# Optimization experiments

Hardware: AMD Instinct MI355X
Metric: run time of the kernel (lower is better)

## Reference

```python
import jax, jax.numpy as jnp
import numpy as np

B, N, C1 = 4, 4096, 58
K = 32
RADIUS = 0.3
CIN = C1 + 6  # xyz(3) + centered grouped_xyz(3) + feature(C1)
OUT_DIMS = [64, 64, 128]
EPS = 1e-5


def setup_inputs() -> dict:
    key = jax.random.key(0)
    ks = jax.random.split(key, 8)
    inp = {
        "feature": jax.random.normal(ks[0], (B, N, C1), dtype=jnp.float32),
        "xyz": jax.random.uniform(ks[1], (B, N, 3), dtype=jnp.float32),
    }
    dims = [CIN] + OUT_DIMS
    for i in range(len(OUT_DIMS)):
        inp[f"W{i}"] = jax.random.normal(ks[2 + i], (dims[i + 1], dims[i]), dtype=jnp.float32) * 0.05
        inp[f"g{i}"] = jnp.ones((dims[i + 1],), dtype=jnp.float32)
        inp[f"b{i}"] = jnp.zeros((dims[i + 1],), dtype=jnp.float32)
    return inp


def ball_query(xyz, radius, k):
    # xyz: (B,N,3) -> grouped neighbor indices (B,N,K), repo semantics:
    # indices with dist > radius set to N, sorted, first K taken, pads replaced by first valid index.
    n = xyz.shape[1]
    sq = jnp.sum((xyz[:, :, None, :] - xyz[:, None, :, :]) ** 2, axis=-1)  # (B,N,N)
    ar = jnp.arange(n, dtype=jnp.int32)[None, None, :]
    inds = jnp.where(sq > radius * radius, n, ar)
    inds = jnp.sort(inds, axis=-1)[:, :, :k]  # (B,N,K)
    first = inds[:, :, :1]
    return jnp.where(inds == n, first, inds)


def group_norm(x, gamma, beta, groups):
    # x: (B,C,K,N); normalize per (group of channels x all spatial)
    b, c, k, n = x.shape
    xg = x.reshape(b, groups, -1)
    mu = jnp.mean(xg, axis=-1, keepdims=True)
    var = jnp.var(xg, axis=-1, keepdims=True)
    xg = (xg - mu) * jax.lax.rsqrt(var + EPS)
    x = xg.reshape(b, c, k, n)
    return x * gamma[None, :, None, None] + beta[None, :, None, None]


def reference(feature, xyz, W0, g0, b0, W1, g1, b1, W2, g2, b2):
    inds = ball_query(xyz, RADIUS, K)  # (B,N,K) int
    gather = jax.vmap(lambda arr, idx: arr[idx])  # per-batch fancy gather
    grouped_xyz = gather(xyz, inds) - xyz[:, :, None, :]        # (B,N,K,3) centered
    grouped_feat = gather(feature, inds)                        # (B,N,K,C1)
    center = jnp.broadcast_to(xyz[:, :, None, :], (B, N, K, 3))  # repeated query xyz
    new_points = jnp.concatenate([center, grouped_xyz, grouped_feat], axis=-1)  # (B,N,K,CIN)

    x = new_points  # layout handled inside einsum: torch permute(0,3,2,1) -> (B,C,K,N)
    params = [(W0, g0, b0), (W1, g1, b1), (W2, g2, b2)]
    first = True
    for (w, g, b_), od in zip(params, OUT_DIMS):
        if first:
            x = jnp.einsum('bnkc,oc->bokn', x, w)  # conv1x1, no bias
            first = False
        else:
            x = jnp.einsum('bikn,oi->bokn', x, w)
        x = group_norm(x, g, b_, od // 32)
        x = jax.nn.relu(x)
    return jnp.max(x, axis=2)  # (B, C2, N)
```

## Files before the change

### kernel.cpp

```cpp
#include <hip/hip_runtime.h>
#include <stdint.h>

#define B_ 4
#define N_ 4096
#define C1_ 58
#define K_ 32
#define EPS_ 1e-5f

typedef __attribute__((ext_vector_type(8))) short bf16x8;
typedef __attribute__((ext_vector_type(4))) float f32x4;

static __device__ __forceinline__ float bf2f(unsigned short u){
  return __uint_as_float(((unsigned int)u) << 16);
}
static __device__ __forceinline__ unsigned short f2bf(float f){
  unsigned int x = __float_as_uint(f);
  x = (x + 0x7FFFu + ((x >> 16) & 1u)) >> 16;
  return (unsigned short)x;
}

__global__ __launch_bounds__(256) void ball_kernel(const float* __restrict__ xyz,
                                                   int* __restrict__ inds){
  const int wid  = (blockIdx.x * 256 + threadIdx.x) >> 6;
  const int lane = threadIdx.x & 63;
  const int b = wid >> 12;
  const int n = wid & (N_ - 1);
  const float* xb = xyz + (size_t)b * N_ * 3;
  const float qx = xb[n*3+0], qy = xb[n*3+1], qz = xb[n*3+2];
  const float R2 = (float)(0.3 * 0.3);
  int* outp = inds + (size_t)wid * K_;
  int cnt = 0;
  int first = -1;
  for (int j0 = 0; j0 < N_ && cnt < K_; j0 += 64){
    const int j = j0 + lane;
    float dx = xb[j*3+0] - qx;
    float dy = xb[j*3+1] - qy;
    float dz = xb[j*3+2] - qz;
    float s = __fadd_rn(__fadd_rn(__fmul_rn(dx,dx), __fmul_rn(dy,dy)), __fmul_rn(dz,dz));
    bool p = (s <= R2);
    unsigned long long mask = __ballot(p);
    if (p){
      int pos = cnt + __popcll(mask & ((1ull << lane) - 1ull));
      if (pos < K_) outp[pos] = j;
    }
    if (first < 0 && mask) first = j0 + __builtin_ctzll(mask);
    cnt += __popcll(mask);
  }
  if (lane < K_ && lane >= cnt) outp[lane] = first;
}

__global__ __launch_bounds__(256)
void pq_kernel(const float* __restrict__ feature, const float* __restrict__ xyz,
               const float* __restrict__ W0g, const float* __restrict__ W2g,
               float* __restrict__ P, unsigned short* __restrict__ Q,
               unsigned short* __restrict__ W2bf)
{
  __shared__ float W0l[64 * 65];
  __shared__ float vql[32][64];
  const int t = threadIdx.x, bid = blockIdx.x;

  if (bid == 0){
    for (int i = t; i < 128 * 64; i += 256) W2bf[i] = f2bf(W2g[i]);
  }
  #pragma unroll
  for (int i = 0; i < 16; ++i){
    int idx = i * 256 + t;
    W0l[(idx >> 6) * 65 + (idx & 63)] = W0g[idx];
  }
  const int gpt0 = bid * 32;
  const int b = gpt0 >> 12;
  const size_t pb = (size_t)b * N_;
  #pragma unroll
  for (int i = 0; i < 8; ++i){
    int task = i * 256 + t;
    int r = task >> 6, c = task & 63;
    int n = (gpt0 + r) & (N_ - 1);
    float val = 0.f;
    if (c < 3)       val = xyz[(pb + n) * 3 + c];
    else if (c < 61) val = feature[(pb + n) * C1_ + (c - 3)];
    vql[r][c] = val;
  }
  __syncthreads();

  const int o = t & 63;
  const int r0 = t >> 6;
  #pragma unroll
  for (int it = 0; it < 8; ++it){
    int r = r0 + it * 4;
    float q0 = 0.f, q1 = 0.f;
    #pragma unroll
    for (int i = 0; i < 60; i += 2){
      q0 = fmaf(W0l[o*65 + 3 + i],     vql[r][i],     q0);
      q1 = fmaf(W0l[o*65 + 3 + i + 1], vql[r][i + 1], q1);
    }
    q0 = fmaf(W0l[o*65 + 3 + 60], vql[r][60], q0);
    float qv = q0 + q1;
    float p = 0.f;
    #pragma unroll
    for (int c = 0; c < 3; ++c)
      p = fmaf(W0l[o*65 + c] - W0l[o*65 + c + 3], vql[r][c], p);
    size_t gpt = (size_t)gpt0 + r;
    P[gpt * 64 + o] = p;
    Q[gpt * 64 + o] = f2bf(qv);
  }
}

__global__ __launch_bounds__(256)
void stats0_kernel(const int* __restrict__ inds, const float* __restrict__ P,
                   const unsigned short* __restrict__ Q, float* __restrict__ partials)
{
  const int t = threadIdx.x, bid = blockIdx.x;
  const size_t row0 = (size_t)bid * 1024;
  const int c8 = t & 7;
  float s = 0.f, q = 0.f;
  for (int i = 0; i < 32; ++i){
    size_t task = (size_t)i * 256 + t;
    size_t row = row0 + (task >> 3);
    int idx = inds[row];
    size_t pt = row >> 5;
    size_t qpt = ((row >> 17) << 12) + idx;
    const float4* pp = (const float4*)(P + pt * 64 + c8 * 8);
    float4 pa = pp[0], pb = pp[1];
    bf16x8 qv = *(const bf16x8*)(Q + qpt * 64 + c8 * 8);
    float pv[8] = {pa.x, pa.y, pa.z, pa.w, pb.x, pb.y, pb.z, pb.w};
    #pragma unroll
    for (int j = 0; j < 8; ++j){
      float y = pv[j] + bf2f((unsigned short)qv[j]);
      s += y; q = fmaf(y, y, q);
    }
  }
  s += __shfl_xor(s, 1, 64);  q += __shfl_xor(q, 1, 64);
  s += __shfl_xor(s, 2, 64);  q += __shfl_xor(q, 2, 64);
  s += __shfl_xor(s, 8, 64);  q += __shfl_xor(q, 8, 64);
  s += __shfl_xor(s, 16, 64); q += __shfl_xor(q, 16, 64);
  s += __shfl_xor(s, 32, 64); q += __shfl_xor(q, 32, 64);
  const int lane = t & 63, w = t >> 6;
  float* out = partials + ((size_t)bid * 4 + w) * 4;
  if (lane == 0){ out[0] = s; out[1] = q; }
  if (lane == 4){ out[2] = s; out[3] = q; }
}

template<int DEPTH>
__global__ __launch_bounds__(512)
void conv_chain(const int* __restrict__ inds, const float* __restrict__ P,
                const unsigned short* __restrict__ Q,
                const float* __restrict__ sc0, const float* __restrict__ sb0,
                const float* __restrict__ W1g, const unsigned short* __restrict__ W2bf,
                const float* __restrict__ sc1, const float* __restrict__ sb1,
                float* __restrict__ partials, float* __restrict__ ymax,
                float* __restrict__ ymin)
{
  constexpr int NGF = (DEPTH == 2) ? 4 : 2;
  constexpr int NG2 = NGF * 2;
  __shared__ unsigned short W1l[64 * 64];
  __shared__ unsigned short Xl[256 * 64];
  __shared__ float spart[8][NG2];

  const int t = threadIdx.x, bid = blockIdx.x;
  const size_t row0 = (size_t)bid * 256;
  const int b = bid >> 9;
  const int lane = t & 63, w = t >> 6;
  const int col = lane & 15, quad = lane >> 4;
  const int c8 = t & 7;

  float s0r[8], b0r[8];
  #pragma unroll
  for (int j = 0; j < 8; ++j){
    s0r[j] = sc0[b * 64 + c8 * 8 + j];
    b0r[j] = sb0[b * 64 + c8 * 8 + j];
  }
  float s1r[4], b1r[4];
  if constexpr (DEPTH == 2){
    #pragma unroll
    for (int nt = 0; nt < 4; ++nt){
      s1r[nt] = sc1[b * 64 + nt * 16 + col];
      b1r[nt] = sb1[b * 64 + nt * 16 + col];
    }
  }

  {
    int ch = t >> 3, c = t & 7;
    const float* wr = W1g + ch * 64 + c * 8;
    bf16x8 v;
    #pragma unroll
    for (int j = 0; j < 8; ++j) v[j] = (short)f2bf(wr[j]);
    *(bf16x8*)&W1l[ch * 64 + ((c ^ (ch & 7)) * 8)] = v;
  }

  #pragma unroll
  for (int i = 0; i < 4; ++i){
    int task = i * 512 + t;
    int r = task >> 3;
    size_t row = row0 + r;
    int idx = inds[row];
    size_t pt = row >> 5;
    size_t qpt = ((row >> 17) << 12) + idx;
    const float4* pp = (const float4*)(P + pt * 64 + c8 * 8);
    float4 pa = pp[0], pb = pp[1];
    bf16x8 qv = *(const bf16x8*)(Q + qpt * 64 + c8 * 8);
    float pv[8] = {pa.x, pa.y, pa.z, pa.w, pb.x, pb.y, pb.z, pb.w};
    bf16x8 v;
    #pragma unroll
    for (int j = 0; j < 8; ++j){
      float y = pv[j] + bf2f((unsigned short)qv[j]);
      float a = fmaf(y, s0r[j], b0r[j]);
      a = fmaxf(a, 0.f);
      v[j] = (short)f2bf(a);
    }
    *(bf16x8*)&Xl[r * 64 + ((c8 ^ (r & 7)) * 8)] = v;
  }
  __syncthreads();

  bf16x8 afr[2][2];
  #pragma unroll
  for (int mi = 0; mi < 2; ++mi){
    int r = w * 32 + mi * 16 + col;
    #pragma unroll
    for (int kt = 0; kt < 2; ++kt)
      afr[mi][kt] = *(const bf16x8*)&Xl[r * 64 + (((kt * 4 + quad) ^ (r & 7)) * 8)];
  }
  f32x4 acc1[2][4];
  #pragma unroll
  for (int mi = 0; mi < 2; ++mi)
    #pragma unroll
    for (int nt = 0; nt < 4; ++nt) acc1[mi][nt] = (f32x4){0.f,0.f,0.f,0.f};
  #pragma unroll
  for (int kt = 0; kt < 2; ++kt)
    #pragma unroll
    for (int nt = 0; nt < 4; ++nt){
      int ch = nt * 16 + col;
      bf16x8 bfr = *(const bf16x8*)&W1l[ch * 64 + (((kt * 4 + quad) ^ (ch & 7)) * 8)];
      #pragma unroll
      for (int mi = 0; mi < 2; ++mi)
        acc1[mi][nt] = __builtin_amdgcn_mfma_f32_16x16x32_bf16(afr[mi][kt], bfr, acc1[mi][nt], 0, 0, 0);
    }

  float sg[NGF], qg[NGF];
  #pragma unroll
  for (int g = 0; g < NGF; ++g){ sg[g] = 0.f; qg[g] = 0.f; }

  if constexpr (DEPTH == 1){
    #pragma unroll
    for (int mi = 0; mi < 2; ++mi)
      #pragma unroll
      for (int nt = 0; nt < 4; ++nt)
        #pragma unroll
        for (int rg = 0; rg < 4; ++rg){
          float y = acc1[mi][nt][rg];
          sg[nt >> 1] += y;
          qg[nt >> 1] = fmaf(y, y, qg[nt >> 1]);
        }
  } else {
    #pragma unroll
    for (int mi = 0; mi < 2; ++mi)
      #pragma unroll
      for (int nt = 0; nt < 4; ++nt)
        #pragma unroll
        for (int rg = 0; rg < 4; ++rg){
          int r = w * 32 + mi * 16 + quad * 4 + rg;
          int ch = nt * 16 + col;
          float v = fmaf(acc1[mi][nt][rg], s1r[nt], b1r[nt]);
          v = fmaxf(v, 0.f);
          Xl[r * 64 + (((ch >> 3) ^ (r & 7)) * 8) + (ch & 7)] = f2bf(v);
        }

    #pragma unroll
    for (int mi = 0; mi < 2; ++mi){
      int r = w * 32 + mi * 16 + col;
      #pragma unroll
      for (int kt = 0; kt < 2; ++kt)
        afr[mi][kt] = *(const bf16x8*)&Xl[r * 64 + (((kt * 4 + quad) ^ (r & 7)) * 8)];
    }
    f32x4 acc2[2][8];
    #pragma unroll
    for (int mi = 0; mi < 2; ++mi)
      #pragma unroll
      for (int nt = 0; nt < 8; ++nt) acc2[mi][nt] = (f32x4){0.f,0.f,0.f,0.f};
    #pragma unroll
    for (int kt = 0; kt < 2; ++kt)
      #pragma unroll
      for (int nt = 0; nt < 8; ++nt){
        int ch = nt * 16 + col;
        bf16x8 bfr = *(const bf16x8*)&W2bf[ch * 64 + (kt * 4 + quad) * 8];
        #pragma unroll
        for (int mi = 0; mi < 2; ++mi)
          acc2[mi][nt] = __builtin_amdgcn_mfma_f32_16x16x32_bf16(afr[mi][kt], bfr, acc2[mi][nt], 0, 0, 0);
      }

    #pragma unroll
    for (int mi = 0; mi < 2; ++mi)
      #pragma unroll
      for (int nt = 0; nt < 8; ++nt)
        #pragma unroll
        for (int rg = 0; rg < 4; ++rg){
          float y = acc2[mi][nt][rg];
          sg[nt >> 1] += y;
          qg[nt >> 1] = fmaf(y, y, qg[nt >> 1]);
        }

    float cmx[8], cmn[8];
    #pragma unroll
    for (int nt = 0; nt < 8; ++nt){
      float mx = acc2[0][nt][0], mn = acc2[0][nt][0];
      #pragma unroll
      for (int mi = 0; mi < 2; ++mi)
        #pragma unroll
        for (int rg = 0; rg < 4; ++rg){
          float y = acc2[mi][nt][rg];
          mx = fmaxf(mx, y); mn = fminf(mn, y);
        }
      mx = fmaxf(mx, __shfl_xor(mx, 16, 64));
      mx = fmaxf(mx, __shfl_xor(mx, 32, 64));
      mn = fminf(mn, __shfl_xor(mn, 16, 64));
      mn = fminf(mn, __shfl_xor(mn, 32, 64));
      cmx[nt] = mx; cmn[nt] = mn;
    }
    if (quad == 0){
      size_t pt = (row0 >> 5) + w;
      #pragma unroll
      for (int nt = 0; nt < 8; ++nt){
        ymax[pt * 128 + nt * 16 + col] = cmx[nt];
        ymin[pt * 128 + nt * 16 + col] = cmn[nt];
      }
    }
  }

  #pragma unroll
  for (int g = 0; g < NGF; ++g){
    #pragma unroll
    for (int off = 32; off > 0; off >>= 1){
      sg[g] += __shfl_down(sg[g], off, 64);
      qg[g] += __shfl_down(qg[g], off, 64);
    }
  }
  if (lane == 0){
    #pragma unroll
    for (int g = 0; g < NGF; ++g){
      spart[w][g * 2 + 0] = sg[g];
      spart[w][g * 2 + 1] = qg[g];
    }
  }
  __syncthreads();
  if (t < NG2){
    float v = 0.f;
    #pragma unroll
    for (int ww = 0; ww < 8; ++ww) v += spart[ww][t];
    partials[(size_t)bid * NG2 + t] = v;
  }
}

template<int NCH, int NPER>
__global__ __launch_bounds__(256)
void finalize_kernel(const float* __restrict__ partials,
                     const float* __restrict__ g, const float* __restrict__ bb,
                     float* __restrict__ sc, float* __restrict__ sb){
  constexpr int NG2 = (NCH / 32) * 2;
  constexpr int NSLOTS = 4 * NG2;
  constexpr int TPS = 256 / NSLOTS;
  __shared__ float st[NSLOTS];
  const int t = threadIdx.x;
  const int slot = t / TPS, j = t % TPS;
  const int b = slot / NG2, idx = slot % NG2;
  float acc = 0.f;
  #pragma unroll
  for (int i = 0; i < NPER / TPS; ++i)
    acc += partials[((size_t)b * NPER + j + i * TPS) * NG2 + idx];
  #pragma unroll
  for (int off = TPS >> 1; off > 0; off >>= 1)
    acc += __shfl_down(acc, off, 64);
  if (j == 0) st[slot] = acc;
  __syncthreads();
  for (int c0 = t; c0 < 4 * NCH; c0 += 256){
    int b2 = c0 / NCH, c = c0 % NCH, grp = c >> 5;
    float s = st[b2 * NG2 + grp * 2 + 0], q = st[b2 * NG2 + grp * 2 + 1];
    const float cnt = 4194304.f;
    float mean = s / cnt;
    float var = q / cnt - mean * mean;
    float rstd = 1.f / sqrtf(var + EPS_);
    float scale = rstd * g[c];
    sc[b2 * NCH + c] = scale;
    sb[b2 * NCH + c] = bb[c] - mean * scale;
  }
}

__global__ __launch_bounds__(256)
void out_kernel(const float* __restrict__ ymax, const float* __restrict__ ymin,
                const float* __restrict__ sc2, const float* __restrict__ sb2,
                float* __restrict__ out){
  __shared__ float tile[64 * 129];
  const int t = threadIdx.x;
  const int b = blockIdx.y;
  const int n0 = blockIdx.x * 64;
  const float4* mx4 = (const float4*)(ymax + ((size_t)b * N_ + n0) * 128);
  const float4* mn4 = (const float4*)(ymin + ((size_t)b * N_ + n0) * 128);
  #pragma unroll
  for (int i = 0; i < 8; ++i){
    int e4 = i * 256 + t;
    int nl = e4 >> 5;
    int ch0 = (e4 & 31) * 4;
    float4 vx = mx4[e4], vn = mn4[e4];
    #pragma unroll
    for (int j = 0; j < 4; ++j){
      float slope = sc2[b*128 + ch0 + j];
      float off   = sb2[b*128 + ch0 + j];
      float y = (slope >= 0.f) ? ((const float*)&vx)[j] : ((const float*)&vn)[j];
      float v = fmaf(y, slope, off);
      tile[nl*129 + ch0 + j] = v > 0.f ? v : 0.f;
    }
  }
  __syncthreads();
  const int ch = t >> 1, h = t & 1;
  float* orow = out + ((size_t)b * 128 + ch) * N_ + n0 + h * 32;
  #pragma unroll
  for (int jj = 0; jj < 8; ++jj){
    float4 v;
    #pragma unroll
    for (int c = 0; c < 4; ++c)
      ((float*)&v)[c] = tile[(h*32 + jj*4 + c)*129 + ch];
    ((float4*)orow)[jj] = v;
  }
}

extern "C" void kernel_launch(void* const* d_in, const int* in_sizes, int n_in,
                              void* d_out, int out_size, void* d_ws, size_t ws_size,
                              hipStream_t stream) {
  const float* feature = (const float*)d_in[0];
  const float* xyz     = (const float*)d_in[1];
  const float* W0 = (const float*)d_in[2];
  const float* g0 = (const float*)d_in[3];
  const float* b0 = (const float*)d_in[4];
  const float* W1 = (const float*)d_in[5];
  const float* g1 = (const float*)d_in[6];
  const float* b1 = (const float*)d_in[7];
  const float* W2 = (const float*)d_in[8];
  const float* g2 = (const float*)d_in[9];
  const float* b2 = (const float*)d_in[10];
  float* out = (float*)d_out;

  char* ws = (char*)d_ws;
  const size_t INDS_BYTES = (size_t)B_ * N_ * K_ * sizeof(int);
  const size_t YBYTES     = (size_t)B_ * N_ * 128 * sizeof(float);
  const size_t PBYTES     = (size_t)B_ * N_ * 64 * sizeof(float);
  const size_t QBYTES     = (size_t)B_ * N_ * 64 * 2;
  int* inds            = (int*)ws;
  float* ymax          = (float*)(ws + INDS_BYTES);
  float* ymin          = (float*)(ws + INDS_BYTES + YBYTES);
  float* P             = (float*)(ws + INDS_BYTES + 2 * YBYTES);
  unsigned short* Q    = (unsigned short*)(ws + INDS_BYTES + 2 * YBYTES + PBYTES);
  unsigned short* W2bf = (unsigned short*)(ws + INDS_BYTES + 2 * YBYTES + PBYTES + QBYTES);
  float* p0 = (float*)(ws + INDS_BYTES + 2 * YBYTES + PBYTES + QBYTES + 16384);
  float* p1 = p0 + 2048 * 4;
  float* p2 = p1 + 2048 * 4;
  float* sc0 = p2 + 2048 * 8;
  float* sb0 = sc0 + 256;
  float* sc1 = sb0 + 256;
  float* sb1 = sc1 + 256;
  float* sc2 = sb1 + 256;
  float* sb2 = sc2 + 512;

  ball_kernel<<<B_ * N_ / 4, 256, 0, stream>>>(xyz, inds);
  pq_kernel<<<B_ * N_ / 32, 256, 0, stream>>>(feature, xyz, W0, W2, P, Q, W2bf);

  stats0_kernel<<<B_ * N_ * K_ / 1024, 256, 0, stream>>>(inds, P, Q, p0);
  finalize_kernel<64, 512><<<1, 256, 0, stream>>>(p0, g0, b0, sc0, sb0);

  const int GRID = B_ * N_ * K_ / 256;

  conv_chain<1><<<GRID, 512, 0, stream>>>(
      inds, P, Q, sc0, sb0, W1, nullptr, nullptr, nullptr,
      p1, nullptr, nullptr);
  finalize_kernel<64, 512><<<1, 256, 0, stream>>>(p1, g1, b1, sc1, sb1);

  conv_chain<2><<<GRID, 512, 0, stream>>>(
      inds, P, Q, sc0, sb0, W1, W2bf, sc1, sb1,
      p2, ymax, ymin);
  finalize_kernel<128, 512><<<1, 256, 0, stream>>>(p2, g2, b2, sc2, sb2);

  dim3 ogrid(N_ / 64, B_);
  out_kernel<<<ogrid, 256, 0, stream>>>(ymax, ymin, sc2, sb2, out);
}
```

Baseline: 154.9 us.

## Make conv_chain persistent over four tiles with double-buffered LDS prefetch

Each conv_chain block now handles four 256-row tiles instead of one, which cuts the grid from 2048 to 512 blocks. The next tile's index and Q gathers are issued before the current tile's MFMA work, and its X tile is written into a second LDS buffer afterwards, so gather latency can overlap compute. Per-block partial counts shrink, so the finalize kernels reduce fewer partials. It also switches the bf16 packing to v_cvt_pk_bf16_f32, restructures the loop per mi to cut register pressure, and initializes max/min with sentinels. The trade-offs are double the LDS footprint (about 72KB per block) and fewer blocks, both of which may lower occupancy and parallelism.

```diff
diff --git a/kernel.cpp b/kernel.cpp
--- a/kernel.cpp
+++ b/kernel.cpp
@@ -17,6 +17,11 @@
   unsigned int x = __float_as_uint(f);
   x = (x + 0x7FFFu + ((x >> 16) & 1u)) >> 16;
   return (unsigned short)x;
+}
+static __device__ __forceinline__ unsigned int cvt_pk_bf16(float lo, float hi){
+  unsigned int r;
+  asm("v_cvt_pk_bf16_f32 %0, %1, %2" : "=v"(r) : "v"(lo), "v"(hi));
+  return r;
 }
 
 __global__ __launch_bounds__(256) void ball_kernel(const float* __restrict__ xyz,
@@ -150,15 +155,16 @@
                 float* __restrict__ partials, float* __restrict__ ymax,
                 float* __restrict__ ymin)
 {
+  constexpr int TILES = 4;
   constexpr int NGF = (DEPTH == 2) ? 4 : 2;
   constexpr int NG2 = NGF * 2;
   __shared__ unsigned short W1l[64 * 64];
-  __shared__ unsigned short Xl[256 * 64];
+  __shared__ unsigned short Xl[2][256 * 64];
   __shared__ float spart[8][NG2];
 
   const int t = threadIdx.x, bid = blockIdx.x;
-  const size_t row0 = (size_t)bid * 256;
-  const int b = bid >> 9;
+  const size_t blk_row0 = (size_t)bid * 1024;
+  const int b = bid >> 7;
   const int lane = t & 63, w = t >> 6;
   const int col = lane & 15, quad = lane >> 4;
   const int c8 = t & 7;
@@ -187,142 +193,151 @@
     *(bf16x8*)&W1l[ch * 64 + ((c ^ (ch & 7)) * 8)] = v;
   }
 
-  #pragma unroll
-  for (int i = 0; i < 4; ++i){
-    int task = i * 512 + t;
-    int r = task >> 3;
-    size_t row = row0 + r;
-    int idx = inds[row];
-    size_t pt = row >> 5;
-    size_t qpt = ((row >> 17) << 12) + idx;
-    const float4* pp = (const float4*)(P + pt * 64 + c8 * 8);
-    float4 pa = pp[0], pb = pp[1];
-    bf16x8 qv = *(const bf16x8*)(Q + qpt * 64 + c8 * 8);
-    float pv[8] = {pa.x, pa.y, pa.z, pa.w, pb.x, pb.y, pb.z, pb.w};
-    bf16x8 v;
-    #pragma unroll
-    for (int j = 0; j < 8; ++j){
-      float y = pv[j] + bf2f((unsigned short)qv[j]);
-      float a = fmaf(y, s0r[j], b0r[j]);
-      a = fmaxf(a, 0.f);
-      v[j] = (short)f2bf(a);
-    }
-    *(bf16x8*)&Xl[r * 64 + ((c8 ^ (r & 7)) * 8)] = v;
-  }
-  __syncthreads();
-
-  bf16x8 afr[2][2];
-  #pragma unroll
-  for (int mi = 0; mi < 2; ++mi){
-    int r = w * 32 + mi * 16 + col;
-    #pragma unroll
-    for (int kt = 0; kt < 2; ++kt)
-      afr[mi][kt] = *(const bf16x8*)&Xl[r * 64 + (((kt * 4 + quad) ^ (r & 7)) * 8)];
-  }
-  f32x4 acc1[2][4];
-  #pragma unroll
-  for (int mi = 0; mi < 2; ++mi)
-    #pragma unroll
-    for (int nt = 0; nt < 4; ++nt) acc1[mi][nt] = (f32x4){0.f,0.f,0.f,0.f};
-  #pragma unroll
-  for (int kt = 0; kt < 2; ++kt)
-    #pragma unroll
-    for (int nt = 0; nt < 4; ++nt){
-      int ch = nt * 16 + col;
-      bf16x8 bfr = *(const bf16x8*)&W1l[ch * 64 + (((kt * 4 + quad) ^ (ch & 7)) * 8)];
-      #pragma unroll
-      for (int mi = 0; mi < 2; ++mi)
-        acc1[mi][nt] = __builtin_amdgcn_mfma_f32_16x16x32_bf16(afr[mi][kt], bfr, acc1[mi][nt], 0, 0, 0);
-    }
+  int    idxr[4];
+  bf16x8 qvr[4];
+
+  auto issue = [&](int tile){
+    const size_t row0 = blk_row0 + (size_t)tile * 256;
+    #pragma unroll
+    for (int i = 0; i < 4; ++i)
+      idxr[i] = inds[row0 + ((i * 512 + t) >> 3)];
+    #pragma unroll
+    for (int i = 0; i < 4; ++i){
+      size_t qpt = ((size_t)b << 12) + idxr[i];
+      qvr[i] = *(const bf16x8*)(Q + qpt * 64 + c8 * 8);
+    }
+  };
+
+  auto writeT = [&](int tile, int buf){
+    const size_t row0 = blk_row0 + (size_t)tile * 256;
+    #pragma unroll
+    for (int i = 0; i < 4; ++i){
+      int r = (i * 512 + t) >> 3;
+      size_t pt = (row0 + r) >> 5;
+      const float4* pp = (const float4*)(P + pt * 64 + c8 * 8);
+      float4 pa = pp[0], pb = pp[1];
+      float pv[8] = {pa.x, pa.y, pa.z, pa.w, pb.x, pb.y, pb.z, pb.w};
+      float a[8];
+      #pragma unroll
+      for (int j = 0; j < 8; ++j){
+        float y = pv[j] + bf2f((unsigned short)qvr[i][j]);
+        float v = fmaf(y, s0r[j], b0r[j]);
+        a[j] = fmaxf(v, 0.f);
+      }
+      unsigned int pk[4];
+      #pragma unroll
+      for (int j = 0; j < 4; ++j) pk[j] = cvt_pk_bf16(a[2*j], a[2*j+1]);
+      unsigned int* dst = (unsigned int*)&Xl[buf][r * 64 + ((c8 ^ (r & 7)) * 8)];
+      #pragma unroll
+      for (int j = 0; j < 4; ++j) dst[j] = pk[j];
+    }
+  };
 
   float sg[NGF], qg[NGF];
   #pragma unroll
   for (int g = 0; g < NGF; ++g){ sg[g] = 0.f; qg[g] = 0.f; }
 
-  if constexpr (DEPTH == 1){
-    #pragma unroll
-    for (int mi = 0; mi < 2; ++mi)
-      #pragma unroll
-      for (int nt = 0; nt < 4; ++nt)
-        #pragma unroll
-        for (int rg = 0; rg < 4; ++rg){
-          float y = acc1[mi][nt][rg];
-          sg[nt >> 1] += y;
-          qg[nt >> 1] = fmaf(y, y, qg[nt >> 1]);
+  issue(0);
+  writeT(0, 0);
+
+  for (int tile = 0; tile < TILES; ++tile){
+    const int cur = tile & 1;
+    const size_t row0 = blk_row0 + (size_t)tile * 256;
+    __syncthreads();
+    if (tile + 1 < TILES) issue(tile + 1);
+
+    float cmx[(DEPTH == 2) ? 8 : 1], cmn[(DEPTH == 2) ? 8 : 1];
+    if constexpr (DEPTH == 2){
+      #pragma unroll
+      for (int nt = 0; nt < 8; ++nt){ cmx[nt] = -1e30f; cmn[nt] = 1e30f; }
+    }
+
+    #pragma unroll
+    for (int mi = 0; mi < 2; ++mi){
+      const int r = w * 32 + mi * 16 + col;
+      bf16x8 afr[2];
+      #pragma unroll
+      for (int kt = 0; kt < 2; ++kt)
+        afr[kt] = *(const bf16x8*)&Xl[cur][r * 64 + (((kt * 4 + quad) ^ (r & 7)) * 8)];
+      f32x4 acc1[4];
+      #pragma unroll
+      for (int nt = 0; nt < 4; ++nt) acc1[nt] = (f32x4){0.f,0.f,0.f,0.f};
+      #pragma unroll
+      for (int kt = 0; kt < 2; ++kt)
+        #pragma unroll
+        for (int nt = 0; nt < 4; ++nt){
+          int ch = nt * 16 + col;
+          bf16x8 bfr = *(const bf16x8*)&W1l[ch * 64 + (((kt * 4 + quad) ^ (ch & 7)) * 8)];
+          acc1[nt] = __builtin_amdgcn_mfma_f32_16x16x32_bf16(afr[kt], bfr, acc1[nt], 0, 0, 0);
         }
-  } else {
-    #pragma unroll
-    for (int mi = 0; mi < 2; ++mi)
-      #pragma unroll
-      for (int nt = 0; nt < 4; ++nt)
-        #pragma unroll
-        for (int rg = 0; rg < 4; ++rg){
-          int r = w * 32 + mi * 16 + quad * 4 + rg;
-          int ch = nt * 16 + col;
-          float v = fmaf(acc1[mi][nt][rg], s1r[nt], b1r[nt]);
-          v = fmaxf(v, 0.f);
-          Xl[r * 64 + (((ch >> 3) ^ (r & 7)) * 8) + (ch & 7)] = f2bf(v);
+
+      if constexpr (DEPTH == 1){
+        #pragma unroll
+        for (int nt = 0; nt < 4; ++nt)
+          #pragma unroll
+          for (int rg = 0; rg < 4; ++rg){
+            float y = acc1[nt][rg];
+            sg[nt >> 1] += y;
+            qg[nt >> 1] = fmaf(y, y, qg[nt >> 1]);
+          }
+      } else {
+        #pragma unroll
+        for (int nt = 0; nt < 4; ++nt)
+          #pragma unroll
+          for (int rg = 0; rg < 4; ++rg){
+            int rr = w * 32 + mi * 16 + quad * 4 + rg;
+            int ch = nt * 16 + col;
+            float v = fmaf(acc1[nt][rg], s1r[nt], b1r[nt]);
+            v = fmaxf(v, 0.f);
+            Xl[cur][rr * 64 + (((ch >> 3) ^ (rr & 7)) * 8) + (ch & 7)] = f2bf(v);
+          }
+        bf16x8 a2f[2];
+        #pragma unroll
+        for (int kt = 0; kt < 2; ++kt)
+          a2f[kt] = *(const bf16x8*)&Xl[cur][r * 64 + (((kt * 4 + quad) ^ (r & 7)) * 8)];
+        f32x4 acc2[8];
+        #pragma unroll
+        for (int nt = 0; nt < 8; ++nt) acc2[nt] = (f32x4){0.f,0.f,0.f,0.f};
+        #pragma unroll
+        for (int kt = 0; kt < 2; ++kt)
+          #pragma unroll
+          for (int nt = 0; nt < 8; ++nt){
+            int ch = nt * 16 + col;
+            bf16x8 bfr = *(const bf16x8*)&W2bf[ch * 64 + (kt * 4 + quad) * 8];
+            acc2[nt] = __builtin_amdgcn_mfma_f32_16x16x32_bf16(a2f[kt], bfr, acc2[nt], 0, 0, 0);
+          }
+        #pragma unroll
+        for (int nt = 0; nt < 8; ++nt)
+          #pragma unroll
+          for (int rg = 0; rg < 4; ++rg){
+            float y = acc2[nt][rg];
+            sg[nt >> 1] += y;
+            qg[nt >> 1] = fmaf(y, y, qg[nt >> 1]);
+            cmx[nt] = fmaxf(cmx[nt], y);
+            cmn[nt] = fminf(cmn[nt], y);
+          }
+      }
+    }
+
+    if constexpr (DEPTH == 2){
+      #pragma unroll
+      for (int nt = 0; nt < 8; ++nt){
+        cmx[nt] = fmaxf(cmx[nt], __shfl_xor(cmx[nt], 16, 64));
+        cmx[nt] = fmaxf(cmx[nt], __shfl_xor(cmx[nt], 32, 64));
+        cmn[nt] = fminf(cmn[nt], __shfl_xor(cmn[nt], 16, 64));
+        cmn[nt] = fminf(cmn[nt], __shfl_xor(cmn[nt], 32, 64));
+      }
+      if (quad == 0){
+        size_t pt = (row0 >> 5) + w;
+        #pragma unroll
+        for (int nt = 0; nt < 8; ++nt){
+          ymax[pt * 128 + nt * 16 + col] = cmx[nt];
+          ymin[pt * 128 + nt * 16 + col] = cmn[nt];
         }
-
-    #pragma unroll
-    for (int mi = 0; mi < 2; ++mi){
-      int r = w * 32 + mi * 16 + col;
-      #pragma unroll
-      for (int kt = 0; kt < 2; ++kt)
-        afr[mi][kt] = *(const bf16x8*)&Xl[r * 64 + (((kt * 4 + quad) ^ (r & 7)) * 8)];
-    }
-    f32x4 acc2[2][8];
-    #pragma unroll
-    for (int mi = 0; mi < 2; ++mi)
-      #pragma unroll
-      for (int nt = 0; nt < 8; ++nt) acc2[mi][nt] = (f32x4){0.f,0.f,0.f,0.f};
-    #pragma unroll
-    for (int kt = 0; kt < 2; ++kt)
-      #pragma unroll
-      for (int nt = 0; nt < 8; ++nt){
-        int ch = nt * 16 + col;
-        bf16x8 bfr = *(const bf16x8*)&W2bf[ch * 64 + (kt * 4 + quad) * 8];
-        #pragma unroll
-        for (int mi = 0; mi < 2; ++mi)
-          acc2[mi][nt] = __builtin_amdgcn_mfma_f32_16x16x32_bf16(afr[mi][kt], bfr, acc2[mi][nt], 0, 0, 0);
       }
-
-    #pragma unroll
-    for (int mi = 0; mi < 2; ++mi)
-      #pragma unroll
-      for (int nt = 0; nt < 8; ++nt)
-        #pragma unroll
-        for (int rg = 0; rg < 4; ++rg){
-          float y = acc2[mi][nt][rg];
-          sg[nt >> 1] += y;
-          qg[nt >> 1] = fmaf(y, y, qg[nt >> 1]);
-        }
-
-    float cmx[8], cmn[8];
-    #pragma unroll
-    for (int nt = 0; nt < 8; ++nt){
-      float mx = acc2[0][nt][0], mn = acc2[0][nt][0];
-      #pragma unroll
-      for (int mi = 0; mi < 2; ++mi)
-        #pragma unroll
-        for (int rg = 0; rg < 4; ++rg){
-          float y = acc2[mi][nt][rg];
-          mx = fmaxf(mx, y); mn = fminf(mn, y);
-        }
-      mx = fmaxf(mx, __shfl_xor(mx, 16, 64));
-      mx = fmaxf(mx, __shfl_xor(mx, 32, 64));
-      mn = fminf(mn, __shfl_xor(mn, 16, 64));
-      mn = fminf(mn, __shfl_xor(mn, 32, 64));
-      cmx[nt] = mx; cmn[nt] = mn;
-    }
-    if (quad == 0){
-      size_t pt = (row0 >> 5) + w;
-      #pragma unroll
-      for (int nt = 0; nt < 8; ++nt){
-        ymax[pt * 128 + nt * 16 + col] = cmx[nt];
-        ymin[pt * 128 + nt * 16 + col] = cmn[nt];
-      }
-    }
+    }
+
+    if (tile + 1 < TILES) writeT(tile + 1, cur ^ 1);
   }
 
   #pragma unroll
@@ -450,8 +465,8 @@
   unsigned short* W2bf = (unsigned short*)(ws + INDS_BYTES + 2 * YBYTES + PBYTES + QBYTES);
   float* p0 = (float*)(ws + INDS_BYTES + 2 * YBYTES + PBYTES + QBYTES + 16384);
   float* p1 = p0 + 2048 * 4;
-  float* p2 = p1 + 2048 * 4;
-  float* sc0 = p2 + 2048 * 8;
+  float* p2 = p1 + 512 * 4;
+  float* sc0 = p2 + 512 * 8;
   float* sb0 = sc0 + 256;
   float* sc1 = sb0 + 256;
   float* sb1 = sc1 + 256;
@@ -464,17 +479,17 @@
   stats0_kernel<<<B_ * N_ * K_ / 1024, 256, 0, stream>>>(inds, P, Q, p0);
   finalize_kernel<64, 512><<<1, 256, 0, stream>>>(p0, g0, b0, sc0, sb0);
 
-  const int GRID = B_ * N_ * K_ / 256;
+  const int GRID = 512;
 
   conv_chain<1><<<GRID, 512, 0, stream>>>(
       inds, P, Q, sc0, sb0, W1, nullptr, nullptr, nullptr,
       p1, nullptr, nullptr);
-  finalize_kernel<64, 512><<<1, 256, 0, stream>>>(p1, g1, b1, sc1, sb1);
+  finalize_kernel<64, 128><<<1, 256, 0, stream>>>(p1, g1, b1, sc1, sb1);
 
   conv_chain<2><<<GRID, 512, 0, stream>>>(
       inds, P, Q, sc0, sb0, W1, W2bf, sc1, sb1,
       p2, ymax, ymin);
-  finalize_kernel<128, 512><<<1, 256, 0, stream>>>(p2, g2, b2, sc2, sb2);
+  finalize_kernel<128, 128><<<1, 256, 0, stream>>>(p2, g2, b2, sc2, sb2);
 
   dim3 ogrid(N_ / 64, B_);
   out_kernel<<<ogrid, 256, 0, stream>>>(ymax, ymin, sc2, sb2, out);
```

Result: faster. 144.2 us (-6.8%).
